# Kernel tuning notes

Measured on AMD Instinct MI355X. Metric: run time of the kernel, lower is better.

The kernel has to match this reference:

```python
import jax, jax.numpy as jnp
import numpy as np


def setup_inputs() -> dict:
    key = jax.random.key(0)
    k1, k2 = jax.random.split(key)
    x = jax.random.normal(k1, (32, 112, 112, 64), dtype=jnp.float32)
    kernels = jax.random.normal(k2, (3, 3, 64, 128), dtype=jnp.float32) * 0.05
    biases = jnp.zeros((128,), dtype=jnp.float32)
    return {"x": x, "kernels": kernels, "biases": biases}


def reference(x, kernels, biases):
    # Stride-1 VALID cross-correlation, NHWC input, HWIO kernel -> NHWC output.
    # Matches the original's per-pixel sum(patch * kernel) over all input channels.
    out = jax.lax.conv_general_dilated(
        x, kernels,
        window_strides=(1, 1),
        padding="VALID",
        dimension_numbers=("NHWC", "HWIO", "NHWC"),
    )
    out = out + biases  # broadcast over (B, H_out, W_out, F)
    return jax.nn.relu(out)  # activation=relu per init_kwargs
```

## Files before the change

### kernel.cpp

```cpp
#include <hip/hip_runtime.h>
#include <hip/hip_bf16.h>

typedef __attribute__((ext_vector_type(4))) float f32x4;
typedef __attribute__((ext_vector_type(8))) short bf16x8;
typedef __attribute__((ext_vector_type(8))) unsigned short u16x8;
typedef __attribute__((ext_vector_type(4))) unsigned int u32x4;

#define IH 112
#define IW 112
#define CIN 64
#define COUT 128
#define HOUT 110
#define WOUT 110
#define MTOT 387200
#define NWGF 3520

__device__ __forceinline__ unsigned short f2bf(float f) {
  unsigned int x = __float_as_uint(f);
  x += 0x7fffu + ((x >> 16) & 1u);
  return (unsigned short)(x >> 16);
}

__device__ __forceinline__ unsigned int cvt2(float lo, float hi) {
  union { __hip_bfloat162 h; unsigned int u; } cv;
  cv.h = __float22bfloat162_rn(float2{lo, hi});
  return cv.u;
}

__device__ __forceinline__ void gload16(const unsigned short* g, unsigned short* l) {
  __builtin_amdgcn_global_load_lds(
      (const __attribute__((address_space(1))) void*)g,
      (__attribute__((address_space(3))) void*)l, 16, 0, 0);
}

__global__ void prepack_b_kernel(const float* __restrict__ kern,
                                 unsigned short* __restrict__ bt) {
  int idx = blockIdx.x * 256 + threadIdx.x;
  if (idx >= 9 * 8192) return;
  int tap = idx >> 13;
  int rem = idx & 8191;
  int co = rem >> 6;
  int e = rem & 63;
  int ci = ((e * 2) ^ ((co & 7) << 4)) >> 1;
  bt[idx] = f2bf(kern[(tap * 64 + ci) * COUT + co]);
}

__global__ __launch_bounds__(512, 4)
void conv_fused_kernel(const float* __restrict__ x,
                       const unsigned short* __restrict__ bt,
                       const float* __restrict__ bias,
                       float* __restrict__ out) {
  __shared__ __align__(16) unsigned short Asl[336 * 64];
  __shared__ __align__(16) unsigned short Bs[2][8192];

  const int tid = threadIdx.x;
  const int lane = tid & 63;
  const int wid = tid >> 6;

  const int bid = blockIdx.x;
  const int wg = (bid & 7) * 440 + (bid >> 3);
  const int bb = wg / 110;
  const int ho = wg - bb * 110;

  const int ldsw0 = wid * 1024;
  const int ldsw1 = wid * 1024 + 512;
  const int blin0 = ldsw0 + lane * 8;
  const int blin1 = ldsw1 + lane * 8;

  gload16(bt + blin0, &Bs[0][ldsw0]);
  gload16(bt + blin1, &Bs[0][ldsw1]);

  {
    const float* xbase = x + ((size_t)(bb * IH + ho) * IW) * CIN;
    for (int it = tid; it < 672; it += 512) {
      const int u = it >> 1;
      const int h = it & 1;
      const int kh = u / 112;
      const int p = u - kh * 112;
      const float* src = xbase + (kh * IW + p) * CIN + h * 32;
      const int key = u & 7;
      unsigned short* rowp = Asl + u * 64;
#pragma unroll
      for (int c2 = 0; c2 < 4; ++c2) {
        f32x4 a = *(const f32x4*)(src + c2 * 8);
        f32x4 b = *(const f32x4*)(src + c2 * 8 + 4);
        u32x4 v;
        v[0] = cvt2(a[0], a[1]); v[1] = cvt2(a[2], a[3]);
        v[2] = cvt2(b[0], b[1]); v[3] = cvt2(b[2], b[3]);
        const int c = h * 4 + c2;
        *(u32x4*)(rowp + ((c ^ key) << 3)) = v;
      }
    }
  }
  __syncthreads();

  const int wm = wid >> 1;
  const int wn = wid & 1;
  const int l16 = lane & 15;
  const int lk = lane >> 4;
  const int swzB = (l16 & 7) << 4;

  const int am0 = wm * 32 + l16;
  const int am1 = wm * 32 + 16 + l16;
  const int broff0 = (wn * 64 + 0 + l16) * 64;
  const int broff1 = (wn * 64 + 16 + l16) * 64;
  const int broff2 = (wn * 64 + 32 + l16) * 64;
  const int broff3 = (wn * 64 + 48 + l16) * 64;

  f32x4 acc[2][4];
#pragma unroll
  for (int i = 0; i < 2; ++i)
#pragma unroll
    for (int j = 0; j < 4; ++j)
      acc[i][j] = (f32x4){0.f, 0.f, 0.f, 0.f};

#pragma unroll
  for (int kk = 0; kk < 9; ++kk) {
    if (kk < 8) {
      const int tb = (kk + 1) * 8192;
      unsigned short* bd = Bs[(kk + 1) & 1];
      gload16(bt + tb + blin0, bd + ldsw0);
      gload16(bt + tb + blin1, bd + ldsw1);
    }

    const int kh = kk / 3;
    const int kw = kk - kh * 3;
    int p0 = am0 + kw; if (p0 > 111) p0 = 111;
    int p1 = am1 + kw; if (p1 > 111) p1 = 111;
    const unsigned short* ar0 = Asl + (kh * 112 + p0) * 64;
    const unsigned short* ar1 = Asl + (kh * 112 + p1) * 64;
    const int sz0 = (p0 & 7) << 4;
    const int sz1 = (p1 & 7) << 4;
    const unsigned short* Bc = Bs[kk & 1];

#pragma unroll
    for (int ks = 0; ks < 2; ++ks) {
      const int kb = ks * 64 + lk * 16;
      bf16x8 a0 = *(const bf16x8*)(ar0 + ((kb ^ sz0) >> 1));
      bf16x8 a1 = *(const bf16x8*)(ar1 + ((kb ^ sz1) >> 1));
      const int cbs = (kb ^ swzB) >> 1;
      bf16x8 b0 = *(const bf16x8*)(Bc + broff0 + cbs);
      bf16x8 b1 = *(const bf16x8*)(Bc + broff1 + cbs);
      bf16x8 b2 = *(const bf16x8*)(Bc + broff2 + cbs);
      bf16x8 b3 = *(const bf16x8*)(Bc + broff3 + cbs);
      acc[0][0] = __builtin_amdgcn_mfma_f32_16x16x32_bf16(a0, b0, acc[0][0], 0, 0, 0);
      acc[0][1] = __builtin_amdgcn_mfma_f32_16x16x32_bf16(a0, b1, acc[0][1], 0, 0, 0);
      acc[0][2] = __builtin_amdgcn_mfma_f32_16x16x32_bf16(a0, b2, acc[0][2], 0, 0, 0);
      acc[0][3] = __builtin_amdgcn_mfma_f32_16x16x32_bf16(a0, b3, acc[0][3], 0, 0, 0);
      acc[1][0] = __builtin_amdgcn_mfma_f32_16x16x32_bf16(a1, b0, acc[1][0], 0, 0, 0);
      acc[1][1] = __builtin_amdgcn_mfma_f32_16x16x32_bf16(a1, b1, acc[1][1], 0, 0, 0);
      acc[1][2] = __builtin_amdgcn_mfma_f32_16x16x32_bf16(a1, b2, acc[1][2], 0, 0, 0);
      acc[1][3] = __builtin_amdgcn_mfma_f32_16x16x32_bf16(a1, b3, acc[1][3], 0, 0, 0);
    }

    if (kk < 8) {
      asm volatile("s_waitcnt vmcnt(0)" ::: "memory");
      __builtin_amdgcn_s_barrier();
    }
  }

  const int ncol = wn * 64 + l16;
  const float bv0 = bias[ncol + 0];
  const float bv1 = bias[ncol + 16];
  const float bv2 = bias[ncol + 32];
  const float bv3 = bias[ncol + 48];
  const size_t mbase = (size_t)bb * 12100 + (size_t)ho * 110;
#pragma unroll
  for (int mf = 0; mf < 2; ++mf) {
    const int wo0 = wm * 32 + mf * 16 + lk * 4;
#pragma unroll
    for (int j = 0; j < 4; ++j) {
      const int wo = wo0 + j;
      if (wo < 110) {
        float* orow = out + (mbase + wo) * COUT + ncol;
        orow[0]  = fmaxf(acc[mf][0][j] + bv0, 0.f);
        orow[16] = fmaxf(acc[mf][1][j] + bv1, 0.f);
        orow[32] = fmaxf(acc[mf][2][j] + bv2, 0.f);
        orow[48] = fmaxf(acc[mf][3][j] + bv3, 0.f);
      }
    }
  }
}

__global__ __launch_bounds__(512)
void conv_fallback_kernel(const float* __restrict__ x,
                          const float* __restrict__ kern,
                          const float* __restrict__ bias,
                          float* __restrict__ out) {
  __shared__ __align__(16) unsigned short As[2][128 * 64];
  __shared__ __align__(16) unsigned short Bs[2][128 * 64];

  const int tid = threadIdx.x;
  const int m0 = blockIdx.x * 128;

  const int sr = tid >> 2;
  const int sc = tid & 3;
  const int m = m0 + sr;
  const int wo = m % WOUT;
  const int t1 = m / WOUT;
  const int ho = t1 % HOUT;
  const int b = t1 / HOUT;
  const float* xrow = x + (((b * IH) + ho) * IW + wo) * CIN + sc * 16;
  const int swzS = (sr & 7) << 4;
  const int awoff0 = sr * 64 + ((((sc * 32) + 0) ^ swzS) >> 1);
  const int awoff1 = sr * 64 + ((((sc * 32) + 16) ^ swzS) >> 1);

  const int bci = tid >> 3;
  const int bco = (tid & 7) * 16;

  const int lane = tid & 63;
  const int wid = tid >> 6;
  const int wm = wid >> 1;
  const int wn = wid & 1;
  const int l16 = lane & 15;
  const int lk = lane >> 4;
  const int swzR = (l16 & 7) << 4;

  const int aroff0 = (wm * 32 + 0 + l16) * 64;
  const int aroff1 = (wm * 32 + 16 + l16) * 64;
  const int broff0 = (wn * 64 + 0 + l16) * 64;
  const int broff1 = (wn * 64 + 16 + l16) * 64;
  const int broff2 = (wn * 64 + 32 + l16) * 64;
  const int broff3 = (wn * 64 + 48 + l16) * 64;

  f32x4 acc[2][4];
#pragma unroll
  for (int i = 0; i < 2; ++i)
#pragma unroll
    for (int j = 0; j < 4; ++j)
      acc[i][j] = (f32x4){0.f, 0.f, 0.f, 0.f};

  {
    f32x4 f0 = *(const f32x4*)(xrow + 0);
    f32x4 f1 = *(const f32x4*)(xrow + 4);
    f32x4 f2 = *(const f32x4*)(xrow + 8);
    f32x4 f3 = *(const f32x4*)(xrow + 12);
    u32x4 va, vb;
    va[0] = cvt2(f0[0], f0[1]); va[1] = cvt2(f0[2], f0[3]);
    va[2] = cvt2(f1[0], f1[1]); va[3] = cvt2(f1[2], f1[3]);
    vb[0] = cvt2(f2[0], f2[1]); vb[1] = cvt2(f2[2], f2[3]);
    vb[2] = cvt2(f3[0], f3[1]); vb[3] = cvt2(f3[2], f3[3]);
    *(u32x4*)(As[0] + awoff0) = va;
    *(u32x4*)(As[0] + awoff1) = vb;
    const float* kslab = kern + bci * COUT + bco;
    f32x4 g0 = *(const f32x4*)(kslab + 0);
    f32x4 g1 = *(const f32x4*)(kslab + 4);
    f32x4 g2 = *(const f32x4*)(kslab + 8);
    f32x4 g3 = *(const f32x4*)(kslab + 12);
#pragma unroll
    for (int j = 0; j < 4; ++j) {
      int c0 = bco + j;
      Bs[0][c0 * 64 + (((bci * 2) ^ ((c0 & 7) << 4)) >> 1)] = f2bf(g0[j]);
      int c1 = bco + 4 + j;
      Bs[0][c1 * 64 + (((bci * 2) ^ ((c1 & 7) << 4)) >> 1)] = f2bf(g1[j]);
      int c2 = bco + 8 + j;
      Bs[0][c2 * 64 + (((bci * 2) ^ ((c2 & 7) << 4)) >> 1)] = f2bf(g2[j]);
      int c3 = bco + 12 + j;
      Bs[0][c3 * 64 + (((bci * 2) ^ ((c3 & 7) << 4)) >> 1)] = f2bf(g3[j]);
    }
  }

#pragma unroll
  for (int kk = 0; kk < 9; ++kk) {
    const int cur = kk & 1;
    const int nxt = cur ^ 1;

    f32x4 g0, g1, g2, g3;
    f32x4 h0, h1, h2, h3;
    if (kk < 8) {
      const int kn = kk + 1;
      const int kh2 = kn / 3;
      const int kw2 = kn - kh2 * 3;
      const float* src = xrow + (kh2 * IW + kw2) * CIN;
      g0 = *(const f32x4*)(src + 0);
      g1 = *(const f32x4*)(src + 4);
      g2 = *(const f32x4*)(src + 8);
      g3 = *(const f32x4*)(src + 12);
      const float* kslab = kern + (kn * 64 + bci) * COUT + bco;
      h0 = *(const f32x4*)(kslab + 0);
      h1 = *(const f32x4*)(kslab + 4);
      h2 = *(const f32x4*)(kslab + 8);
      h3 = *(const f32x4*)(kslab + 12);
    }

    __syncthreads();

    const unsigned short* Ac = As[cur];
    const unsigned short* Bc = Bs[cur];
#pragma unroll
    for (int ks = 0; ks < 2; ++ks) {
      const int cbs = ((ks * 64 + lk * 16) ^ swzR) >> 1;
      bf16x8 a0 = *(const bf16x8*)(Ac + aroff0 + cbs);
      bf16x8 a1 = *(const bf16x8*)(Ac + aroff1 + cbs);
      bf16x8 b0 = *(const bf16x8*)(Bc + broff0 + cbs);
      bf16x8 b1 = *(const bf16x8*)(Bc + broff1 + cbs);
      bf16x8 b2 = *(const bf16x8*)(Bc + broff2 + cbs);
      bf16x8 b3 = *(const bf16x8*)(Bc + broff3 + cbs);
      acc[0][0] = __builtin_amdgcn_mfma_f32_16x16x32_bf16(a0, b0, acc[0][0], 0, 0, 0);
      acc[0][1] = __builtin_amdgcn_mfma_f32_16x16x32_bf16(a0, b1, acc[0][1], 0, 0, 0);
      acc[0][2] = __builtin_amdgcn_mfma_f32_16x16x32_bf16(a0, b2, acc[0][2], 0, 0, 0);
      acc[0][3] = __builtin_amdgcn_mfma_f32_16x16x32_bf16(a0, b3, acc[0][3], 0, 0, 0);
      acc[1][0] = __builtin_amdgcn_mfma_f32_16x16x32_bf16(a1, b0, acc[1][0], 0, 0, 0);
      acc[1][1] = __builtin_amdgcn_mfma_f32_16x16x32_bf16(a1, b1, acc[1][1], 0, 0, 0);
      acc[1][2] = __builtin_amdgcn_mfma_f32_16x16x32_bf16(a1, b2, acc[1][2], 0, 0, 0);
      acc[1][3] = __builtin_amdgcn_mfma_f32_16x16x32_bf16(a1, b3, acc[1][3], 0, 0, 0);
    }

    if (kk < 8) {
      u32x4 va, vb;
      va[0] = cvt2(g0[0], g0[1]); va[1] = cvt2(g0[2], g0[3]);
      va[2] = cvt2(g1[0], g1[1]); va[3] = cvt2(g1[2], g1[3]);
      vb[0] = cvt2(g2[0], g2[1]); vb[1] = cvt2(g2[2], g2[3]);
      vb[2] = cvt2(g3[0], g3[1]); vb[3] = cvt2(g3[2], g3[3]);
      *(u32x4*)(As[nxt] + awoff0) = va;
      *(u32x4*)(As[nxt] + awoff1) = vb;
#pragma unroll
      for (int j = 0; j < 4; ++j) {
        int c0 = bco + j;
        Bs[nxt][c0 * 64 + (((bci * 2) ^ ((c0 & 7) << 4)) >> 1)] = f2bf(h0[j]);
        int c1 = bco + 4 + j;
        Bs[nxt][c1 * 64 + (((bci * 2) ^ ((c1 & 7) << 4)) >> 1)] = f2bf(h1[j]);
        int c2 = bco + 8 + j;
        Bs[nxt][c2 * 64 + (((bci * 2) ^ ((c2 & 7) << 4)) >> 1)] = f2bf(h2[j]);
        int c3 = bco + 12 + j;
        Bs[nxt][c3 * 64 + (((bci * 2) ^ ((c3 & 7) << 4)) >> 1)] = f2bf(h3[j]);
      }
    }
  }

  const int ncol = wn * 64 + l16;
  const float bv0 = bias[ncol + 0];
  const float bv1 = bias[ncol + 16];
  const float bv2 = bias[ncol + 32];
  const float bv3 = bias[ncol + 48];
  const int mrow0 = m0 + wm * 32 + lk * 4;
#pragma unroll
  for (int mf = 0; mf < 2; ++mf) {
#pragma unroll
    for (int j = 0; j < 4; ++j) {
      const int row = mrow0 + mf * 16 + j;
      float* orow = out + (size_t)row * COUT + ncol;
      orow[0]  = fmaxf(acc[mf][0][j] + bv0, 0.f);
      orow[16] = fmaxf(acc[mf][1][j] + bv1, 0.f);
      orow[32] = fmaxf(acc[mf][2][j] + bv2, 0.f);
      orow[48] = fmaxf(acc[mf][3][j] + bv3, 0.f);
    }
  }
}

extern "C" void kernel_launch(void* const* d_in, const int* in_sizes, int n_in,
                              void* d_out, int out_size, void* d_ws, size_t ws_size,
                              hipStream_t stream) {
  const float* x = (const float*)d_in[0];
  const float* kern = (const float*)d_in[1];
  const float* bias = (const float*)d_in[2];
  float* out = (float*)d_out;

  const size_t bt_bytes = 9 * 8192 * 2;
  if (d_ws != nullptr && ws_size >= bt_bytes) {
    unsigned short* bt = (unsigned short*)d_ws;
    prepack_b_kernel<<<288, 256, 0, stream>>>(kern, bt);
    conv_fused_kernel<<<NWGF, 512, 0, stream>>>(x, bt, bias, out);
  } else {
    conv_fallback_kernel<<<3025, 512, 0, stream>>>(x, kern, bias, out);
  }
}
```

Before: 111.7 us.

## Load weight fragments directly from global memory instead of LDS double buffer

Removes the LDS double-buffered weight tiles and the per-tap barrier. Each wave now reads its bf16 weight fragments straight from global memory (expected to be served from L2) into registers. The prepack kernel drops the swizzle to match the plain layout. This cuts LDS use and synchronization, which may raise occupancy, but it exposes global load latency inside the tap loop without explicit prefetch.

```diff
diff --git a/kernel.cpp b/kernel.cpp
--- a/kernel.cpp
+++ b/kernel.cpp
@@ -27,12 +27,6 @@
   return cv.u;
 }
 
-__device__ __forceinline__ void gload16(const unsigned short* g, unsigned short* l) {
-  __builtin_amdgcn_global_load_lds(
-      (const __attribute__((address_space(1))) void*)g,
-      (__attribute__((address_space(3))) void*)l, 16, 0, 0);
-}
-
 __global__ void prepack_b_kernel(const float* __restrict__ kern,
                                  unsigned short* __restrict__ bt) {
   int idx = blockIdx.x * 256 + threadIdx.x;
@@ -40,8 +34,7 @@
   int tap = idx >> 13;
   int rem = idx & 8191;
   int co = rem >> 6;
-  int e = rem & 63;
-  int ci = ((e * 2) ^ ((co & 7) << 4)) >> 1;
+  int ci = rem & 63;
   bt[idx] = f2bf(kern[(tap * 64 + ci) * COUT + co]);
 }
 
@@ -51,7 +44,6 @@
                        const float* __restrict__ bias,
                        float* __restrict__ out) {
   __shared__ __align__(16) unsigned short Asl[336 * 64];
-  __shared__ __align__(16) unsigned short Bs[2][8192];
 
   const int tid = threadIdx.x;
   const int lane = tid & 63;
@@ -61,14 +53,6 @@
   const int wg = (bid & 7) * 440 + (bid >> 3);
   const int bb = wg / 110;
   const int ho = wg - bb * 110;
-
-  const int ldsw0 = wid * 1024;
-  const int ldsw1 = wid * 1024 + 512;
-  const int blin0 = ldsw0 + lane * 8;
-  const int blin1 = ldsw1 + lane * 8;
-
-  gload16(bt + blin0, &Bs[0][ldsw0]);
-  gload16(bt + blin1, &Bs[0][ldsw1]);
 
   {
     const float* xbase = x + ((size_t)(bb * IH + ho) * IW) * CIN;
@@ -98,14 +82,11 @@
   const int wn = wid & 1;
   const int l16 = lane & 15;
   const int lk = lane >> 4;
-  const int swzB = (l16 & 7) << 4;
 
   const int am0 = wm * 32 + l16;
   const int am1 = wm * 32 + 16 + l16;
-  const int broff0 = (wn * 64 + 0 + l16) * 64;
-  const int broff1 = (wn * 64 + 16 + l16) * 64;
-  const int broff2 = (wn * 64 + 32 + l16) * 64;
-  const int broff3 = (wn * 64 + 48 + l16) * 64;
+
+  const unsigned short* bq_base = bt + (wn * 64 + l16) * 64 + lk * 8;
 
   f32x4 acc[2][4];
 #pragma unroll
@@ -116,46 +97,51 @@
 
 #pragma unroll
   for (int kk = 0; kk < 9; ++kk) {
-    if (kk < 8) {
-      const int tb = (kk + 1) * 8192;
-      unsigned short* bd = Bs[(kk + 1) & 1];
-      gload16(bt + tb + blin0, bd + ldsw0);
-      gload16(bt + tb + blin1, bd + ldsw1);
-    }
-
     const int kh = kk / 3;
     const int kw = kk - kh * 3;
+
     int p0 = am0 + kw; if (p0 > 111) p0 = 111;
     int p1 = am1 + kw; if (p1 > 111) p1 = 111;
     const unsigned short* ar0 = Asl + (kh * 112 + p0) * 64;
     const unsigned short* ar1 = Asl + (kh * 112 + p1) * 64;
     const int sz0 = (p0 & 7) << 4;
     const int sz1 = (p1 & 7) << 4;
-    const unsigned short* Bc = Bs[kk & 1];
-
-#pragma unroll
-    for (int ks = 0; ks < 2; ++ks) {
-      const int kb = ks * 64 + lk * 16;
+
+    const unsigned short* btap = bq_base + kk * 8192;
+    bf16x8 b00 = *(const bf16x8*)(btap + 0 * 1024 + 0);
+    bf16x8 b01 = *(const bf16x8*)(btap + 1 * 1024 + 0);
+    bf16x8 b02 = *(const bf16x8*)(btap + 2 * 1024 + 0);
+    bf16x8 b03 = *(const bf16x8*)(btap + 3 * 1024 + 0);
+    bf16x8 b10 = *(const bf16x8*)(btap + 0 * 1024 + 32);
+    bf16x8 b11 = *(const bf16x8*)(btap + 1 * 1024 + 32);
+    bf16x8 b12 = *(const bf16x8*)(btap + 2 * 1024 + 32);
+    bf16x8 b13 = *(const bf16x8*)(btap + 3 * 1024 + 32);
+
+    {
+      const int kb = lk * 16;
       bf16x8 a0 = *(const bf16x8*)(ar0 + ((kb ^ sz0) >> 1));
       bf16x8 a1 = *(const bf16x8*)(ar1 + ((kb ^ sz1) >> 1));
-      const int cbs = (kb ^ swzB) >> 1;
-      bf16x8 b0 = *(const bf16x8*)(Bc + broff0 + cbs);
-      bf16x8 b1 = *(const bf16x8*)(Bc + broff1 + cbs);
-      bf16x8 b2 = *(const bf16x8*)(Bc + broff2 + cbs);
-      bf16x8 b3 = *(const bf16x8*)(Bc + broff3 + cbs);
-      acc[0][0] = __builtin_amdgcn_mfma_f32_16x16x32_bf16(a0, b0, acc[0][0], 0, 0, 0);
-      acc[0][1] = __builtin_amdgcn_mfma_f32_16x16x32_bf16(a0, b1, acc[0][1], 0, 0, 0);
-      acc[0][2] = __builtin_amdgcn_mfma_f32_16x16x32_bf16(a0, b2, acc[0][2], 0, 0, 0);
-      acc[0][3] = __builtin_amdgcn_mfma_f32_16x16x32_bf16(a0, b3, acc[0][3], 0, 0, 0);
-      acc[1][0] = __builtin_amdgcn_mfma_f32_16x16x32_bf16(a1, b0, acc[1][0], 0, 0, 0);
-      acc[1][1] = __builtin_amdgcn_mfma_f32_16x16x32_bf16(a1, b1, acc[1][1], 0, 0, 0);
-      acc[1][2] = __builtin_amdgcn_mfma_f32_16x16x32_bf16(a1, b2, acc[1][2], 0, 0, 0);
-      acc[1][3] = __builtin_amdgcn_mfma_f32_16x16x32_bf16(a1, b3, acc[1][3], 0, 0, 0);
-    }
-
-    if (kk < 8) {
-      asm volatile("s_waitcnt vmcnt(0)" ::: "memory");
-      __builtin_amdgcn_s_barrier();
+      acc[0][0] = __builtin_amdgcn_mfma_f32_16x16x32_bf16(a0, b00, acc[0][0], 0, 0, 0);
+      acc[0][1] = __builtin_amdgcn_mfma_f32_16x16x32_bf16(a0, b01, acc[0][1], 0, 0, 0);
+      acc[0][2] = __builtin_amdgcn_mfma_f32_16x16x32_bf16(a0, b02, acc[0][2], 0, 0, 0);
+      acc[0][3] = __builtin_amdgcn_mfma_f32_16x16x32_bf16(a0, b03, acc[0][3], 0, 0, 0);
+      acc[1][0] = __builtin_amdgcn_mfma_f32_16x16x32_bf16(a1, b00, acc[1][0], 0, 0, 0);
+      acc[1][1] = __builtin_amdgcn_mfma_f32_16x16x32_bf16(a1, b01, acc[1][1], 0, 0, 0);
+      acc[1][2] = __builtin_amdgcn_mfma_f32_16x16x32_bf16(a1, b02, acc[1][2], 0, 0, 0);
+      acc[1][3] = __builtin_amdgcn_mfma_f32_16x16x32_bf16(a1, b03, acc[1][3], 0, 0, 0);
+    }
+    {
+      const int kb = 64 + lk * 16;
+      bf16x8 a0 = *(const bf16x8*)(ar0 + ((kb ^ sz0) >> 1));
+      bf16x8 a1 = *(const bf16x8*)(ar1 + ((kb ^ sz1) >> 1));
+      acc[0][0] = __builtin_amdgcn_mfma_f32_16x16x32_bf16(a0, b10, acc[0][0], 0, 0, 0);
+      acc[0][1] = __builtin_amdgcn_mfma_f32_16x16x32_bf16(a0, b11, acc[0][1], 0, 0, 0);
+      acc[0][2] = __builtin_amdgcn_mfma_f32_16x16x32_bf16(a0, b12, acc[0][2], 0, 0, 0);
+      acc[0][3] = __builtin_amdgcn_mfma_f32_16x16x32_bf16(a0, b13, acc[0][3], 0, 0, 0);
+      acc[1][0] = __builtin_amdgcn_mfma_f32_16x16x32_bf16(a1, b10, acc[1][0], 0, 0, 0);
+      acc[1][1] = __builtin_amdgcn_mfma_f32_16x16x32_bf16(a1, b11, acc[1][1], 0, 0, 0);
+      acc[1][2] = __builtin_amdgcn_mfma_f32_16x16x32_bf16(a1, b12, acc[1][2], 0, 0, 0);
+      acc[1][3] = __builtin_amdgcn_mfma_f32_16x16x32_bf16(a1, b13, acc[1][3], 0, 0, 0);
     }
   }
 
```

New measurement: 284.7 us. 155% more time.
